# Optimization experiments

Hardware: AMD Instinct MI355X
Metric: run time of the kernel (lower is better)

Reference implementation:

```python
import jax, jax.numpy as jnp
import numpy as np
from jax import lax

SPARSITY = 0.5  # args.sparsity: fraction of weights KEPT


def get_subnet(scores, k):
    """GetSubnet.forward: sort |scores|, zero lowest (1-k) fraction, one elsewhere."""
    sa = jnp.abs(scores)
    n = sa.size
    j = int((1.0 - k) * n)  # static: number of entries zeroed
    idx = jnp.argsort(sa.ravel())  # ascending, matches torch .sort()
    mask = jnp.zeros((n,), dtype=sa.dtype).at[idx[j:]].set(1.0)
    return mask.reshape(scores.shape)


def masked_conv(x, w, s, b, stride):
    m = get_subnet(s, SPARSITY)
    y = lax.conv_general_dilated(
        x, w * m, window_strides=(stride, stride), padding=((1, 1), (1, 1)),
        dimension_numbers=('NCHW', 'OIHW', 'NCHW'))
    return y + b[None, :, None, None]


def setup_inputs() -> dict:
    key = jax.random.key(0)
    ks = jax.random.split(key, 16)
    def rn(k, shape, scale):
        return jax.random.normal(k, shape, dtype=jnp.float32) * scale
    return {
        'x':   rn(ks[0], (64, 3, 64, 64), 1.0),
        'w1':  rn(ks[1], (128, 3, 3, 3), 0.2),   's1': rn(ks[2], (128, 3, 3, 3), 1.0),   'b1': rn(ks[3], (128,), 0.01),
        'w2':  rn(ks[4], (256, 128, 3, 3), 0.05), 's2': rn(ks[5], (256, 128, 3, 3), 1.0), 'b2': rn(ks[6], (256,), 0.01),
        'w3':  rn(ks[7], (512, 256, 3, 3), 0.03), 's3': rn(ks[8], (512, 256, 3, 3), 1.0), 'b3': rn(ks[9], (512,), 0.01),
        'fw1': rn(ks[10], (1024, 512), 0.05),     'fs1': rn(ks[11], (1024, 512), 1.0),    'fb1': rn(ks[12], (1024,), 0.01),
        'fw2': rn(ks[13], (10, 1024), 0.05),      'fs2': rn(ks[14], (10, 1024), 1.0),     'fb2': rn(ks[15], (10,), 0.01),
    }


def reference(x, w1, s1, b1, w2, s2, b2, w3, s3, b3, fw1, fs1, fb1, fw2, fs2, fb2):
    h = jax.nn.relu(masked_conv(x, w1, s1, b1, stride=1))   # [64,128,64,64]
    h = jax.nn.relu(masked_conv(h, w2, s2, b2, stride=2))   # [64,256,32,32]
    h = jax.nn.relu(masked_conv(h, w3, s3, b3, stride=2))   # [64,512,16,16]
    h = h.mean(axis=(2, 3))                                 # [64,512] global avg pool
    m1 = get_subnet(fs1, SPARSITY)
    h = jax.nn.relu(h @ (fw1 * m1).T + fb1)                 # [64,1024]
    m2 = get_subnet(fs2, SPARSITY)
    return h @ (fw2 * m2).T + fb2                           # [64,10]
```

## Files before the change

kernel.cpp:

```cpp
#include <hip/hip_runtime.h>
#include <stdint.h>


typedef __attribute__((ext_vector_type(8))) short short8;
typedef __attribute__((ext_vector_type(4))) short short4v;
typedef __attribute__((ext_vector_type(4))) float floatx4;

__device__ __forceinline__ unsigned short f2bf(float f) {
    unsigned u = __float_as_uint(f);
    u += 0x7fffu + ((u >> 16) & 1u);
    return (unsigned short)(u >> 16);
}

constexpr unsigned CUM0 = 3456u;
constexpr unsigned CUM1 = 298368u;
constexpr unsigned CUM2 = 1478016u;
constexpr unsigned CUM3 = 2002304u;
constexpr unsigned STOT = 2012544u;
constexpr int NBH = 128;

__device__ __forceinline__ int find_tensor(unsigned idx, unsigned& li) {
    if (idx < CUM0) { li = idx;        return 0; }
    if (idx < CUM1) { li = idx - CUM0; return 1; }
    if (idx < CUM2) { li = idx - CUM1; return 2; }
    if (idx < CUM3) { li = idx - CUM2; return 3; }
    li = idx - CUM3; return 4;
}

__global__ __launch_bounds__(256) void hist8(const float* __restrict__ s0,
                                             const float* __restrict__ s1,
                                             const float* __restrict__ s2,
                                             const float* __restrict__ s3,
                                             const float* __restrict__ s4,
                                             const unsigned* __restrict__ P,
                                             unsigned* __restrict__ partials, int pass) {
    __shared__ unsigned lh[4 * 1280];
    const int tid = threadIdx.x;
    const int wv = tid >> 6;
    for (int i = tid; i < 4 * 1280; i += 256) lh[i] = 0;
    __syncthreads();

    const int hi_sh = 31 - 8 * pass;
    const int bin_sh = 23 - 8 * pass;
    unsigned pref[5];
    #pragma unroll
    for (int t = 0; t < 5; t++) pref[t] = pass ? P[t] : 0u;

    for (unsigned idx = blockIdx.x * 256u + tid; idx < STOT; idx += NBH * 256u) {
        unsigned li; int t = find_tensor(idx, li);
        const float* sp = t == 0 ? s0 : t == 1 ? s1 : t == 2 ? s2 : t == 3 ? s3 : s4;
        unsigned key = __float_as_uint(sp[li]) & 0x7fffffffu;
        if ((key >> hi_sh) == pref[t]) {
            unsigned bin = (pass == 3) ? (key & 127u) : ((key >> bin_sh) & 255u);
            atomicAdd(&lh[wv * 1280 + (unsigned)t * 256u + bin], 1u);
        }
    }
    __syncthreads();
    for (int i = tid; i < 1280; i += 256)
        partials[(size_t)blockIdx.x * 1280 + i] =
            lh[i] + lh[1280 + i] + lh[2560 + i] + lh[3840 + i];
}

__global__ __launch_bounds__(256) void find8(const unsigned* __restrict__ partials,
                                             unsigned* __restrict__ P,
                                             unsigned* __restrict__ targ, int pass) {
    const int t = blockIdx.x;
    const int tid = threadIdx.x;
    __shared__ unsigned bins[256];
    unsigned s = 0;
    for (int b = 0; b < NBH; b++) s += partials[(size_t)b * 1280 + t * 256 + tid];
    bins[tid] = s;
    __syncthreads();
    if (tid == 0) {
        unsigned n = t == 0 ? 3456u : t == 1 ? 294912u : t == 2 ? 1179648u
                   : t == 3 ? 524288u : 10240u;
        unsigned target = (pass == 0) ? (n >> 1) : targ[t];
        unsigned cum = 0; int b = 0;
        for (; b < 256; b++) { unsigned c = bins[b]; if (cum + c > target) break; cum += c; }
        targ[t] = target - cum;
        unsigned prev = (pass == 0) ? 0u : P[t];
        P[t] = (prev << ((pass == 3) ? 7 : 8)) | (unsigned)b;
    }
}

__global__ void mask_reorder(const float* __restrict__ w0, const float* __restrict__ w1,
                             const float* __restrict__ w2, const float* __restrict__ w3,
                             const float* __restrict__ w4,
                             const float* __restrict__ s0, const float* __restrict__ s1,
                             const float* __restrict__ s2, const float* __restrict__ s3,
                             const float* __restrict__ s4,
                             const unsigned* __restrict__ T,
                             float* __restrict__ wm1,
                             unsigned short* __restrict__ A2,
                             unsigned short* __restrict__ A3,
                             float* __restrict__ fwm1, float* __restrict__ fwm2,
                             float* __restrict__ pooled) {
    unsigned idx = blockIdx.x * 256u + threadIdx.x;
    if (idx >= STOT) return;
    if (idx < 32768u) pooled[idx] = 0.f;
    unsigned li; int t = find_tensor(idx, li);
    const float* sp = t == 0 ? s0 : t == 1 ? s1 : t == 2 ? s2 : t == 3 ? s3 : s4;
    const float* wp = t == 0 ? w0 : t == 1 ? w1 : t == 2 ? w2 : t == 3 ? w3 : w4;
    unsigned key = __float_as_uint(sp[li]) & 0x7fffffffu;
    float val = (key >= T[t]) ? wp[li] : 0.f;
    if (t == 0) {
        wm1[li] = val;
    } else if (t == 1) {
        unsigned k = li / 1152u, r = li - k * 1152u;
        unsigned c = r / 9u, e = r - c * 9u;
        A2[((size_t)e * 256u + k) * 128u + c] = f2bf(val);
    } else if (t == 2) {
        unsigned k = li / 2304u, r = li - k * 2304u;
        unsigned c = r / 9u, e = r - c * 9u;
        A3[((size_t)e * 512u + k) * 256u + c] = f2bf(val);
    } else if (t == 3) {
        fwm1[li] = val;
    } else {
        fwm2[li] = val;
    }
}

template <int C, int H, int W, int K, int TX, int TY, int KT>
__global__ __launch_bounds__(TX* TY) void conv_direct(const float* __restrict__ in,
                                                      const float* __restrict__ wm,
                                                      const float* __restrict__ bias,
                                                      unsigned short* __restrict__ out) {
    constexpr int TILW = TX * 2, TILH = TY * 2;
    constexpr int ITW = TILW + 2, ITH = TILH + 2;
    constexpr int NTHREADS = TX * TY;
    constexpr int NLOAD = (ITH * ITW + NTHREADS - 1) / NTHREADS;
    constexpr int KG = K / KT;

    __shared__ float sIn[ITH * ITW];
    __shared__ float sW[9 * KT];

    const int tid = threadIdx.x;
    const int tx = tid % TX, ty = tid / TX;
    const int kg = blockIdx.z % KG, n = blockIdx.z / KG;
    const int ox0 = blockIdx.x * TILW, oy0 = blockIdx.y * TILH;
    const int ix0 = ox0 - 1, iy0 = oy0 - 1;

    const float* inN = in + (size_t)n * C * H * W;
    const float* wkg = wm + (size_t)kg * KT * C * 9;

    int goff[NLOAD];
    #pragma unroll
    for (int i = 0; i < NLOAD; i++) {
        int idx = tid + i * NTHREADS;
        if (idx < ITH * ITW) {
            int r = idx / ITW, col = idx % ITW;
            int gy = iy0 + r, gx = ix0 + col;
            goff[i] = (gy >= 0 && gy < H && gx >= 0 && gx < W) ? (gy * W + gx) : -1;
        } else goff[i] = -2;
    }

    float acc[2][2][KT];
    #pragma unroll
    for (int py = 0; py < 2; py++)
        #pragma unroll
        for (int px = 0; px < 2; px++)
            #pragma unroll
            for (int j = 0; j < KT; j++) acc[py][px][j] = 0.f;

    for (int c = 0; c < C; c++) {
        const float* inC = inN + (size_t)c * H * W;
        #pragma unroll
        for (int i = 0; i < NLOAD; i++) {
            int g = goff[i];
            if (g >= -1) sIn[tid + i * NTHREADS] = (g >= 0) ? inC[g] : 0.f;
        }
        for (int i = tid; i < 9 * KT; i += NTHREADS) {
            int e = i / KT, j = i % KT;
            sW[i] = wkg[j * C * 9 + c * 9 + e];
        }
        __syncthreads();

        float vin[4][4];
        const float* base = &sIn[(ty * 2) * ITW + tx * 2];
        #pragma unroll
        for (int r = 0; r < 4; r++)
            #pragma unroll
            for (int cc = 0; cc < 4; cc++) vin[r][cc] = base[r * ITW + cc];

        #pragma unroll
        for (int e = 0; e < 9; e++) {
            const int dy = e / 3, dx = e % 3;
            #pragma unroll
            for (int j = 0; j < KT; j++) {
                float wv = sW[e * KT + j];
                #pragma unroll
                for (int py = 0; py < 2; py++)
                    #pragma unroll
                    for (int px = 0; px < 2; px++)
                        acc[py][px][j] = fmaf(vin[py + dy][px + dx], wv, acc[py][px][j]);
            }
        }
        __syncthreads();
    }

    float bj[KT];
    #pragma unroll
    for (int j = 0; j < KT; j++) bj[j] = bias[kg * KT + j];
    #pragma unroll
    for (int py = 0; py < 2; py++)
        #pragma unroll
        for (int px = 0; px < 2; px++) {
            int oy = oy0 + ty * 2 + py, ox = ox0 + tx * 2 + px;
            short8 v;
            #pragma unroll
            for (int j = 0; j < KT; j++) {
                float t = acc[py][px][j] + bj[j];
                v[j] = (short)f2bf(t > 0.f ? t : 0.f);
            }
            *(short8*)(out + ((size_t)(n * H + oy) * W + ox) * K + kg * KT) = v;
        }
}

template <int C, int H, int W, int KOUT, bool POOL>
__global__ __launch_bounds__(256) void conv_mfma(const unsigned short* __restrict__ in,
                                                 const unsigned short* __restrict__ A,
                                                 const float* __restrict__ bias,
                                                 void* __restrict__ outv) {
    constexpr int OH = H / 2, OW = W / 2;
    constexpr int PR = 128 / OW;
    constexpr int RH = 2 * PR + 1;
    constexpr int IW = W + 1;
    constexpr int NC = C / 32;
    constexpr int PSTR = 40;
    constexpr int NSLOT = RH * IW * 4;
    constexpr int SLMAX = (NSLOT + 255) / 256;

    __shared__ unsigned short sIn[RH * IW * PSTR];

    const int tid = threadIdx.x;
    const int lane = tid & 63;
    const int wv = tid >> 6;
    const int l15 = lane & 15;
    const int quad = lane >> 4;
    const int pt = blockIdx.x, kb = blockIdx.y, n = blockIdx.z;
    const int k0 = kb * 128;
    const int oy0 = pt * PR;
    const int g0y = 2 * oy0 - 1;
    const int mw = wv * 32;

    int goff[SLMAX], slds[SLMAX];
    #pragma unroll
    for (int i = 0; i < SLMAX; i++) {
        int s = tid + i * 256;
        if (s < NSLOT) {
            int q = s & 3, pix = s >> 2;
            int ix = pix % IW, iy = pix / IW;
            int gy = g0y + iy, gx = ix - 1;
            slds[i] = pix * PSTR + q * 8;
            goff[i] = (gy >= 0 && gy < H && gx >= 0) ? ((gy * W + gx) * C + q * 8) : -1;
        } else { goff[i] = -2; slds[i] = 0; }
    }

    int pB[8];
    #pragma unroll
    for (int fn = 0; fn < 8; fn++) {
        int p = fn * 16 + l15;
        int oyl = p / OW, oxl = p % OW;
        pB[fn] = (oyl * 2 * IW + oxl * 2) * PSTR + quad * 8;
    }

    const unsigned short* inN = in + (size_t)n * H * W * C;

    floatx4 acc[2][8];
    #pragma unroll
    for (int fm = 0; fm < 2; fm++)
        #pragma unroll
        for (int fn = 0; fn < 8; fn++) acc[fm][fn] = (floatx4){0.f, 0.f, 0.f, 0.f};

    for (int cc = 0; cc < NC; cc++) {
        __syncthreads();
        const int cof = cc * 32;
        #pragma unroll
        for (int i = 0; i < SLMAX; i++) {
            int g = goff[i];
            if (g >= 0) {
                *(short8*)&sIn[slds[i]] = *(const short8*)(inN + g + cof);
            } else if (g == -1 && cc == 0) {
                *(short8*)&sIn[slds[i]] = (short8){0, 0, 0, 0, 0, 0, 0, 0};
            }
        }
        __syncthreads();

        const unsigned short* Abase = A + (size_t)(k0 + mw + l15) * C + cof + quad * 8;
        const size_t estr = (size_t)KOUT * C;

        short8 a0 = *(const short8*)(Abase);
        short8 a1 = *(const short8*)(Abase + 16 * C);

        #pragma unroll 1
        for (int e = 0; e < 9; e++) {
            short8 ac0 = a0, ac1 = a1;
            if (e < 8) {
                a0 = *(const short8*)(Abase + (size_t)(e + 1) * estr);
                a1 = *(const short8*)(Abase + (size_t)(e + 1) * estr + 16 * C);
            }
            const int dy = e / 3, dx = e - dy * 3;
            const int boff = (dy * IW + dx) * PSTR;
            short8 bfr[8];
            #pragma unroll
            for (int fn = 0; fn < 8; fn++)
                bfr[fn] = *(const short8*)&sIn[pB[fn] + boff];
            #pragma unroll
            for (int fn = 0; fn < 8; fn++) {
                acc[0][fn] = __builtin_amdgcn_mfma_f32_16x16x32_bf16(ac0, bfr[fn], acc[0][fn], 0, 0, 0);
                acc[1][fn] = __builtin_amdgcn_mfma_f32_16x16x32_bf16(ac1, bfr[fn], acc[1][fn], 0, 0, 0);
            }
        }
    }

    if (!POOL) {
        unsigned short* out = (unsigned short*)outv;
        #pragma unroll
        for (int fm = 0; fm < 2; fm++) {
            const int k4 = k0 + mw + fm * 16 + quad * 4;
            float b0 = bias[k4], b1 = bias[k4 + 1], b2 = bias[k4 + 2], b3 = bias[k4 + 3];
            #pragma unroll
            for (int fn = 0; fn < 8; fn++) {
                int p = fn * 16 + l15;
                int oy = oy0 + p / OW, ox = p % OW;
                float v0 = acc[fm][fn][0] + b0, v1 = acc[fm][fn][1] + b1;
                float v2 = acc[fm][fn][2] + b2, v3 = acc[fm][fn][3] + b3;
                short4v v;
                v[0] = (short)f2bf(v0 > 0.f ? v0 : 0.f);
                v[1] = (short)f2bf(v1 > 0.f ? v1 : 0.f);
                v[2] = (short)f2bf(v2 > 0.f ? v2 : 0.f);
                v[3] = (short)f2bf(v3 > 0.f ? v3 : 0.f);
                *(short4v*)(out + ((size_t)(n * OH + oy) * OW + ox) * KOUT + k4) = v;
            }
        }
    } else {
        float* out = (float*)outv;
        #pragma unroll
        for (int fm = 0; fm < 2; fm++) {
            #pragma unroll
            for (int reg = 0; reg < 4; reg++) {
                int k = k0 + mw + fm * 16 + quad * 4 + reg;
                float bv = bias[k];
                float s = 0.f;
                #pragma unroll
                for (int fn = 0; fn < 8; fn++) {
                    float v = acc[fm][fn][reg] + bv;
                    s += v > 0.f ? v : 0.f;
                }
                s += __shfl_xor(s, 1); s += __shfl_xor(s, 2);
                s += __shfl_xor(s, 4); s += __shfl_xor(s, 8);
                if (l15 == 0) atomicAdd(&out[n * KOUT + k], s * (1.0f / (OH * OW)));
            }
        }
    }
}

__global__ void fc1_kernel(const float* __restrict__ pooled, const float* __restrict__ w,
                           const float* __restrict__ b, float* __restrict__ out) {
    int t = blockIdx.x * 256 + threadIdx.x;
    int o = t & 1023, n = t >> 10;
    const float4* w4 = (const float4*)(w + (size_t)o * 512);
    const float4* p4 = (const float4*)(pooled + (size_t)n * 512);
    float acc = 0.f;
    for (int i = 0; i < 128; i++) {
        float4 a = p4[i], ww = w4[i];
        acc += a.x * ww.x + a.y * ww.y + a.z * ww.z + a.w * ww.w;
    }
    acc += b[o];
    out[t] = acc > 0.f ? acc : 0.f;
}

__global__ void fc2_kernel(const float* __restrict__ h, const float* __restrict__ w,
                           const float* __restrict__ b, float* __restrict__ out) {
    int n = blockIdx.x, tid = threadIdx.x;
    __shared__ float redw[40];
    const float4* h4 = (const float4*)(h + (size_t)n * 1024);
    float4 a = h4[tid];
    for (int o = 0; o < 10; o++) {
        const float4* w4 = (const float4*)(w + (size_t)o * 1024);
        float4 ww = w4[tid];
        float v = a.x * ww.x + a.y * ww.y + a.z * ww.z + a.w * ww.w;
        for (int off = 32; off > 0; off >>= 1) v += __shfl_down(v, off);
        if ((tid & 63) == 0) redw[o * 4 + (tid >> 6)] = v;
    }
    __syncthreads();
    if (tid < 10) {
        float s = redw[tid * 4] + redw[tid * 4 + 1] + redw[tid * 4 + 2] + redw[tid * 4 + 3] + b[tid];
        out[n * 10 + tid] = s;
    }
}

extern "C" void kernel_launch(void* const* d_in, const int* in_sizes, int n_in,
                              void* d_out, int out_size, void* d_ws, size_t ws_size,
                              hipStream_t stream) {
    const float* x   = (const float*)d_in[0];
    const float* w1  = (const float*)d_in[1];
    const float* s1  = (const float*)d_in[2];
    const float* b1  = (const float*)d_in[3];
    const float* w2  = (const float*)d_in[4];
    const float* s2  = (const float*)d_in[5];
    const float* b2  = (const float*)d_in[6];
    const float* w3  = (const float*)d_in[7];
    const float* s3  = (const float*)d_in[8];
    const float* b3  = (const float*)d_in[9];
    const float* fw1 = (const float*)d_in[10];
    const float* fs1 = (const float*)d_in[11];
    const float* fb1 = (const float*)d_in[12];
    const float* fw2 = (const float*)d_in[13];
    const float* fs2 = (const float*)d_in[14];
    const float* fb2 = (const float*)d_in[15];
    float* out = (float*)d_out;

    char* ws = (char*)d_ws;
    size_t off = 0;
    auto alloc = [&](size_t bytes) -> char* {
        char* p = ws + off;
        off = (off + bytes + 255) & ~(size_t)255;
        return p;
    };
    unsigned* partials = (unsigned*)alloc((size_t)NBH * 1280 * 4);
    unsigned* P        = (unsigned*)alloc(64);
    unsigned* targ     = (unsigned*)alloc(64);
    float* wm1  = (float*)alloc(3456ull * 4);
    float* fwm1 = (float*)alloc(524288ull * 4);
    float* fwm2 = (float*)alloc(10240ull * 4);
    unsigned short* A2 = (unsigned short*)alloc(294912ull * 2);
    unsigned short* A3 = (unsigned short*)alloc(1179648ull * 2);
    unsigned short* h1 = (unsigned short*)alloc(33554432ull * 2);
    unsigned short* h2 = (unsigned short*)alloc(16777216ull * 2);
    float* pooled = (float*)alloc(32768ull * 4);
    float* fc1h   = (float*)alloc(65536ull * 4);
    if (off > ws_size) return;

    for (int pass = 0; pass < 4; pass++) {
        hist8<<<NBH, 256, 0, stream>>>(s1, s2, s3, fs1, fs2, P, partials, pass);
        find8<<<5, 256, 0, stream>>>(partials, P, targ, pass);
    }
    int gs = (STOT + 255) / 256;
    mask_reorder<<<gs, 256, 0, stream>>>(w1, w2, w3, fw1, fw2, s1, s2, s3, fs1, fs2, P,
                                         wm1, A2, A3, fwm1, fwm2, pooled);

    conv_direct<3, 64, 64, 128, 16, 16, 8>
        <<<dim3(2, 2, 64 * 16), 256, 0, stream>>>(x, wm1, b1, h1);
    conv_mfma<128, 64, 64, 256, false>
        <<<dim3(8, 2, 64), 256, 0, stream>>>(h1, A2, b2, h2);
    conv_mfma<256, 32, 32, 512, true>
        <<<dim3(2, 4, 64), 256, 0, stream>>>(h2, A3, b3, pooled);

    fc1_kernel<<<256, 256, 0, stream>>>(pooled, fwm1, fb1, fc1h);
    fc2_kernel<<<64, 256, 0, stream>>>(fc1h, fwm2, fb2, out);
}
```

Before: 454.0 us.

## Fuse histogram and bin-find via last-block ticket; fuse FC1 and FC2

Replaces the per-pass hist8+find8 pair with one kernel that accumulates block histograms into a global histogram with atomics, and lets the last block to finish (chosen by a done counter) pick the radix bin. Grid size rises from 128 to 512 blocks, and a memset clears the counters. The two FC layers become one kernel per batch row that keeps the pooled vector and hidden activations in shared memory. This removes four launches, the partials round-trip and the fc1h buffer. In exchange, the FC1 weight matrix is re-read by only 64 blocks with less parallelism, and the histogram adds global atomic contention.

```diff
diff --git a/kernel.cpp b/kernel.cpp
--- a/kernel.cpp
+++ b/kernel.cpp
@@ -17,7 +17,7 @@
 constexpr unsigned CUM2 = 1478016u;
 constexpr unsigned CUM3 = 2002304u;
 constexpr unsigned STOT = 2012544u;
-constexpr int NBH = 128;
+constexpr int NBH = 512;
 
 __device__ __forceinline__ int find_tensor(unsigned idx, unsigned& li) {
     if (idx < CUM0) { li = idx;        return 0; }
@@ -27,14 +27,18 @@
     li = idx - CUM3; return 4;
 }
 
-__global__ __launch_bounds__(256) void hist8(const float* __restrict__ s0,
-                                             const float* __restrict__ s1,
-                                             const float* __restrict__ s2,
-                                             const float* __restrict__ s3,
-                                             const float* __restrict__ s4,
-                                             const unsigned* __restrict__ P,
-                                             unsigned* __restrict__ partials, int pass) {
+__global__ __launch_bounds__(256) void histfind(const float* __restrict__ s0,
+                                                const float* __restrict__ s1,
+                                                const float* __restrict__ s2,
+                                                const float* __restrict__ s3,
+                                                const float* __restrict__ s4,
+                                                unsigned* __restrict__ ghist4,
+                                                unsigned* __restrict__ done,
+                                                unsigned* __restrict__ P,
+                                                unsigned* __restrict__ targ,
+                                                int pass) {
     __shared__ unsigned lh[4 * 1280];
+    __shared__ unsigned sticket;
     const int tid = threadIdx.x;
     const int wv = tid >> 6;
     for (int i = tid; i < 4 * 1280; i += 256) lh[i] = 0;
@@ -46,7 +50,7 @@
     #pragma unroll
     for (int t = 0; t < 5; t++) pref[t] = pass ? P[t] : 0u;
 
-    for (unsigned idx = blockIdx.x * 256u + tid; idx < STOT; idx += NBH * 256u) {
+    for (unsigned idx = blockIdx.x * 256u + tid; idx < STOT; idx += (unsigned)NBH * 256u) {
         unsigned li; int t = find_tensor(idx, li);
         const float* sp = t == 0 ? s0 : t == 1 ? s1 : t == 2 ? s2 : t == 3 ? s3 : s4;
         unsigned key = __float_as_uint(sp[li]) & 0x7fffffffu;
@@ -56,30 +60,35 @@
         }
     }
     __syncthreads();
-    for (int i = tid; i < 1280; i += 256)
-        partials[(size_t)blockIdx.x * 1280 + i] =
-            lh[i] + lh[1280 + i] + lh[2560 + i] + lh[3840 + i];
-}
-
-__global__ __launch_bounds__(256) void find8(const unsigned* __restrict__ partials,
-                                             unsigned* __restrict__ P,
-                                             unsigned* __restrict__ targ, int pass) {
-    const int t = blockIdx.x;
-    const int tid = threadIdx.x;
-    __shared__ unsigned bins[256];
-    unsigned s = 0;
-    for (int b = 0; b < NBH; b++) s += partials[(size_t)b * 1280 + t * 256 + tid];
-    bins[tid] = s;
+
+    unsigned* gh = ghist4 + pass * 1280;
+    for (int i = tid; i < 1280; i += 256) {
+        unsigned v = lh[i] + lh[1280 + i] + lh[2560 + i] + lh[3840 + i];
+        if (v) atomicAdd(&gh[i], v);
+    }
     __syncthreads();
     if (tid == 0) {
-        unsigned n = t == 0 ? 3456u : t == 1 ? 294912u : t == 2 ? 1179648u
-                   : t == 3 ? 524288u : 10240u;
-        unsigned target = (pass == 0) ? (n >> 1) : targ[t];
-        unsigned cum = 0; int b = 0;
-        for (; b < 256; b++) { unsigned c = bins[b]; if (cum + c > target) break; cum += c; }
-        targ[t] = target - cum;
-        unsigned prev = (pass == 0) ? 0u : P[t];
-        P[t] = (prev << ((pass == 3) ? 7 : 8)) | (unsigned)b;
+        __threadfence();
+        sticket = atomicAdd(&done[pass], 1u);
+    }
+    __syncthreads();
+
+    if (sticket == (unsigned)(NBH - 1)) {
+        for (int i = tid; i < 1280; i += 256)
+            lh[i] = atomicAdd(&gh[i], 0u);
+        __syncthreads();
+        if (tid < 5) {
+            int t = tid;
+            unsigned n = t == 0 ? 3456u : t == 1 ? 294912u : t == 2 ? 1179648u
+                       : t == 3 ? 524288u : 10240u;
+            unsigned target = (pass == 0) ? (n >> 1) : targ[t];
+            const unsigned* bins = &lh[t * 256];
+            unsigned cum = 0; int b = 0;
+            for (; b < 256; b++) { unsigned c = bins[b]; if (cum + c > target) break; cum += c; }
+            targ[t] = target - cum;
+            unsigned prev = (pass == 0) ? 0u : P[t];
+            P[t] = (prev << ((pass == 3) ? 7 : 8)) | (unsigned)b;
+        }
     }
 }
 
@@ -355,38 +364,50 @@
     }
 }
 
-__global__ void fc1_kernel(const float* __restrict__ pooled, const float* __restrict__ w,
-                           const float* __restrict__ b, float* __restrict__ out) {
-    int t = blockIdx.x * 256 + threadIdx.x;
-    int o = t & 1023, n = t >> 10;
-    const float4* w4 = (const float4*)(w + (size_t)o * 512);
-    const float4* p4 = (const float4*)(pooled + (size_t)n * 512);
-    float acc = 0.f;
-    for (int i = 0; i < 128; i++) {
-        float4 a = p4[i], ww = w4[i];
-        acc += a.x * ww.x + a.y * ww.y + a.z * ww.z + a.w * ww.w;
-    }
-    acc += b[o];
-    out[t] = acc > 0.f ? acc : 0.f;
-}
-
-__global__ void fc2_kernel(const float* __restrict__ h, const float* __restrict__ w,
-                           const float* __restrict__ b, float* __restrict__ out) {
-    int n = blockIdx.x, tid = threadIdx.x;
+__global__ __launch_bounds__(256) void fc_fused(const float* __restrict__ pooled,
+                                                const float* __restrict__ w1v,
+                                                const float* __restrict__ b1v,
+                                                const float* __restrict__ w2v,
+                                                const float* __restrict__ b2v,
+                                                float* __restrict__ out) {
+    const int n = blockIdx.x, tid = threadIdx.x;
+    __shared__ float sp[512];
+    __shared__ float sh[1024];
     __shared__ float redw[40];
-    const float4* h4 = (const float4*)(h + (size_t)n * 1024);
-    float4 a = h4[tid];
+
+    {
+        float2 v = *(const float2*)(pooled + (size_t)n * 512 + tid * 2);
+        sp[tid * 2] = v.x; sp[tid * 2 + 1] = v.y;
+    }
+    __syncthreads();
+
+    #pragma unroll
+    for (int j = 0; j < 4; j++) {
+        int o = tid + j * 256;
+        const float4* w4 = (const float4*)(w1v + (size_t)o * 512);
+        float acc = 0.f;
+        for (int i = 0; i < 128; i++) {
+            float4 ww = w4[i];
+            acc += sp[i * 4] * ww.x + sp[i * 4 + 1] * ww.y
+                 + sp[i * 4 + 2] * ww.z + sp[i * 4 + 3] * ww.w;
+        }
+        acc += b1v[o];
+        sh[o] = acc > 0.f ? acc : 0.f;
+    }
+    __syncthreads();
+
     for (int o = 0; o < 10; o++) {
-        const float4* w4 = (const float4*)(w + (size_t)o * 1024);
+        const float4* w4 = (const float4*)(w2v + (size_t)o * 1024);
         float4 ww = w4[tid];
-        float v = a.x * ww.x + a.y * ww.y + a.z * ww.z + a.w * ww.w;
+        float v = sh[tid * 4] * ww.x + sh[tid * 4 + 1] * ww.y
+                + sh[tid * 4 + 2] * ww.z + sh[tid * 4 + 3] * ww.w;
         for (int off = 32; off > 0; off >>= 1) v += __shfl_down(v, off);
         if ((tid & 63) == 0) redw[o * 4 + (tid >> 6)] = v;
     }
     __syncthreads();
     if (tid < 10) {
-        float s = redw[tid * 4] + redw[tid * 4 + 1] + redw[tid * 4 + 2] + redw[tid * 4 + 3] + b[tid];
-        out[n * 10 + tid] = s;
+        out[n * 10 + tid] = redw[tid * 4] + redw[tid * 4 + 1]
+                          + redw[tid * 4 + 2] + redw[tid * 4 + 3] + b2v[tid];
     }
 }
 
@@ -418,9 +439,10 @@
         off = (off + bytes + 255) & ~(size_t)255;
         return p;
     };
-    unsigned* partials = (unsigned*)alloc((size_t)NBH * 1280 * 4);
-    unsigned* P        = (unsigned*)alloc(64);
-    unsigned* targ     = (unsigned*)alloc(64);
+    unsigned* ghist = (unsigned*)alloc((4 * 1280 + 16) * 4);
+    unsigned* done  = ghist + 4 * 1280;
+    unsigned* P     = (unsigned*)alloc(64);
+    unsigned* targ  = (unsigned*)alloc(64);
     float* wm1  = (float*)alloc(3456ull * 4);
     float* fwm1 = (float*)alloc(524288ull * 4);
     float* fwm2 = (float*)alloc(10240ull * 4);
@@ -429,13 +451,13 @@
     unsigned short* h1 = (unsigned short*)alloc(33554432ull * 2);
     unsigned short* h2 = (unsigned short*)alloc(16777216ull * 2);
     float* pooled = (float*)alloc(32768ull * 4);
-    float* fc1h   = (float*)alloc(65536ull * 4);
     if (off > ws_size) return;
 
-    for (int pass = 0; pass < 4; pass++) {
-        hist8<<<NBH, 256, 0, stream>>>(s1, s2, s3, fs1, fs2, P, partials, pass);
-        find8<<<5, 256, 0, stream>>>(partials, P, targ, pass);
-    }
+    (void)hipMemsetAsync(ghist, 0, (4 * 1280 + 16) * 4, stream);
+
+    for (int pass = 0; pass < 4; pass++)
+        histfind<<<NBH, 256, 0, stream>>>(s1, s2, s3, fs1, fs2, ghist, done, P, targ, pass);
+
     int gs = (STOT + 255) / 256;
     mask_reorder<<<gs, 256, 0, stream>>>(w1, w2, w3, fw1, fw2, s1, s2, s3, fs1, fs2, P,
                                          wm1, A2, A3, fwm1, fwm2, pooled);
@@ -447,6 +469,5 @@
     conv_mfma<256, 32, 32, 512, true>
         <<<dim3(2, 4, 64), 256, 0, stream>>>(h2, A3, b3, pooled);
 
-    fc1_kernel<<<256, 256, 0, stream>>>(pooled, fwm1, fb1, fc1h);
-    fc2_kernel<<<64, 256, 0, stream>>>(fc1h, fwm2, fb2, out);
-}
+    fc_fused<<<64, 256, 0, stream>>>(pooled, fwm1, fb1, fwm2, fb2, out);
+}
```

Result: slower. 469.3 us (+3.4%).

## Use three-pass 11/11/9-bit radix select with global atomic histograms

Applied to the files above, without the earlier changes.

Replaces the four-pass 8-bit radix selection of the per-tensor median threshold with three passes of 11, 11 and 9 bits. Each pass reads all scores once, so dropping a pass removes one full read of about 8 MB of scores plus one hist/find launch pair. Per-block partial histograms are no longer written out and reduced; each block instead flushes its nonzero shared bins into a global histogram with atomics, which is zeroed by a memset. The larger bin count removes the per-wave privatised shared histograms, which can raise shared-atomic contention, and the find step now scans in two levels.

```diff
diff --git a/kernel.cpp b/kernel.cpp
--- a/kernel.cpp
+++ b/kernel.cpp
@@ -27,59 +27,72 @@
     li = idx - CUM3; return 4;
 }
 
-__global__ __launch_bounds__(256) void hist8(const float* __restrict__ s0,
-                                             const float* __restrict__ s1,
-                                             const float* __restrict__ s2,
-                                             const float* __restrict__ s3,
-                                             const float* __restrict__ s4,
-                                             const unsigned* __restrict__ P,
-                                             unsigned* __restrict__ partials, int pass) {
-    __shared__ unsigned lh[4 * 1280];
+__global__ __launch_bounds__(256) void hist11(const float* __restrict__ s0,
+                                              const float* __restrict__ s1,
+                                              const float* __restrict__ s2,
+                                              const float* __restrict__ s3,
+                                              const float* __restrict__ s4,
+                                              const unsigned* __restrict__ P,
+                                              unsigned* __restrict__ ghist, int pass) {
+    __shared__ unsigned lh[10240];
     const int tid = threadIdx.x;
-    const int wv = tid >> 6;
-    for (int i = tid; i < 4 * 1280; i += 256) lh[i] = 0;
+    const int NB = (pass == 2) ? 512 : 2048;
+    for (int i = tid; i < NB * 5; i += 256) lh[i] = 0;
     __syncthreads();
 
-    const int hi_sh = 31 - 8 * pass;
-    const int bin_sh = 23 - 8 * pass;
     unsigned pref[5];
     #pragma unroll
     for (int t = 0; t < 5; t++) pref[t] = pass ? P[t] : 0u;
+    const int fsh = (pass == 1) ? 20 : 9;
 
     for (unsigned idx = blockIdx.x * 256u + tid; idx < STOT; idx += NBH * 256u) {
         unsigned li; int t = find_tensor(idx, li);
         const float* sp = t == 0 ? s0 : t == 1 ? s1 : t == 2 ? s2 : t == 3 ? s3 : s4;
         unsigned key = __float_as_uint(sp[li]) & 0x7fffffffu;
-        if ((key >> hi_sh) == pref[t]) {
-            unsigned bin = (pass == 3) ? (key & 127u) : ((key >> bin_sh) & 255u);
-            atomicAdd(&lh[wv * 1280 + (unsigned)t * 256u + bin], 1u);
+        bool ok = (pass == 0) || ((key >> fsh) == pref[t]);
+        if (ok) {
+            unsigned bin = (pass == 0) ? (key >> 20)
+                         : (pass == 1) ? ((key >> 9) & 2047u)
+                                       : (key & 511u);
+            atomicAdd(&lh[(unsigned)t * NB + bin], 1u);
         }
     }
     __syncthreads();
-    for (int i = tid; i < 1280; i += 256)
-        partials[(size_t)blockIdx.x * 1280 + i] =
-            lh[i] + lh[1280 + i] + lh[2560 + i] + lh[3840 + i];
-}
-
-__global__ __launch_bounds__(256) void find8(const unsigned* __restrict__ partials,
-                                             unsigned* __restrict__ P,
-                                             unsigned* __restrict__ targ, int pass) {
+    const int goff = (pass == 0) ? 0 : (pass == 1) ? 10240 : 20480;
+    for (int i = tid; i < NB * 5; i += 256) {
+        unsigned v = lh[i];
+        if (v) atomicAdd(&ghist[goff + i], v);
+    }
+}
+
+__global__ __launch_bounds__(256) void find11(const unsigned* __restrict__ ghist,
+                                              unsigned* __restrict__ P,
+                                              unsigned* __restrict__ targ, int pass) {
     const int t = blockIdx.x;
     const int tid = threadIdx.x;
-    __shared__ unsigned bins[256];
+    const int NB = (pass == 2) ? 512 : 2048;
+    const int goff = (pass == 0) ? 0 : (pass == 1) ? 10240 : 20480;
+    const int seg = NB / 256;
+    __shared__ unsigned bins[2048];
+    __shared__ unsigned part[256];
+    for (int i = tid; i < NB; i += 256) bins[i] = ghist[goff + t * NB + i];
+    __syncthreads();
     unsigned s = 0;
-    for (int b = 0; b < NBH; b++) s += partials[(size_t)b * 1280 + t * 256 + tid];
-    bins[tid] = s;
+    for (int j = 0; j < seg; j++) s += bins[tid * seg + j];
+    part[tid] = s;
     __syncthreads();
     if (tid == 0) {
         unsigned n = t == 0 ? 3456u : t == 1 ? 294912u : t == 2 ? 1179648u
                    : t == 3 ? 524288u : 10240u;
         unsigned target = (pass == 0) ? (n >> 1) : targ[t];
-        unsigned cum = 0; int b = 0;
-        for (; b < 256; b++) { unsigned c = bins[b]; if (cum + c > target) break; cum += c; }
+        unsigned cum = 0; int q = 0;
+        for (; q < 256; q++) { unsigned c = part[q]; if (cum + c > target) break; cum += c; }
+        int b = q * seg;
+        for (;; b++) { unsigned c = bins[b]; if (cum + c > target) break; cum += c; }
         targ[t] = target - cum;
-        unsigned prev = (pass == 0) ? 0u : P[t];
-        P[t] = (prev << ((pass == 3) ? 7 : 8)) | (unsigned)b;
+        if (pass == 0)      P[t] = (unsigned)b;
+        else if (pass == 1) P[t] = (P[t] << 11) | (unsigned)b;
+        else                P[t] = (P[t] << 9) | (unsigned)b;
     }
 }
 
@@ -418,9 +431,9 @@
         off = (off + bytes + 255) & ~(size_t)255;
         return p;
     };
-    unsigned* partials = (unsigned*)alloc((size_t)NBH * 1280 * 4);
-    unsigned* P        = (unsigned*)alloc(64);
-    unsigned* targ     = (unsigned*)alloc(64);
+    unsigned* ghist = (unsigned*)alloc(23040ull * 4);
+    unsigned* P     = (unsigned*)alloc(64);
+    unsigned* targ  = (unsigned*)alloc(64);
     float* wm1  = (float*)alloc(3456ull * 4);
     float* fwm1 = (float*)alloc(524288ull * 4);
     float* fwm2 = (float*)alloc(10240ull * 4);
@@ -432,9 +445,11 @@
     float* fc1h   = (float*)alloc(65536ull * 4);
     if (off > ws_size) return;
 
-    for (int pass = 0; pass < 4; pass++) {
-        hist8<<<NBH, 256, 0, stream>>>(s1, s2, s3, fs1, fs2, P, partials, pass);
-        find8<<<5, 256, 0, stream>>>(partials, P, targ, pass);
+    (void)hipMemsetAsync(ghist, 0, 23040ull * 4, stream);
+
+    for (int pass = 0; pass < 3; pass++) {
+        hist11<<<NBH, 256, 0, stream>>>(s1, s2, s3, fs1, fs2, P, ghist, pass);
+        find11<<<5, 256, 0, stream>>>(ghist, P, targ, pass);
     }
     int gs = (STOT + 255) / 256;
     mask_reorder<<<gs, 256, 0, stream>>>(w1, w2, w3, fw1, fw2, s1, s2, s3, fs1, fs2, P,
```

Result: faster. 438.0 us (-3.5%).
